# Kernel optimization log

Measured on AMD Instinct MI355X. Metric: run time of the kernel, lower is better.

## Reference

```python
import jax, jax.numpy as jnp
import numpy as np

GAMMA_MIN, GAMMA_MAX = 0.15, 1.0
ALPHA_CAP = 1.0
EPS_L2 = 1e-8
EPS_RMS = 1e-6


def _rmsnorm(x, w):
    return x * jax.lax.rsqrt(jnp.mean(x * x, axis=-1, keepdims=True) + EPS_RMS) * w


def _l2norm(x):
    n = jnp.linalg.norm(x, axis=-1, keepdims=True)
    return x / jnp.maximum(n, EPS_L2)


def _causal_conv(h, kernel):
    # depthwise-shared causal conv over time: out[b,t] = sum_j kernel[j] * h[b, t-j]
    K = kernel.shape[0]
    S = h.shape[1]
    hp = jnp.pad(h, ((0, 0), (K - 1, 0), (0, 0)))
    out = jnp.zeros_like(h)
    for j in range(K):  # K is a small fixed constant (4)
        out = out + kernel[j] * hp[:, K - 1 - j:K - 1 - j + S, :]
    return out


def setup_inputs() -> dict:
    B, S, D, R, K = 8, 1024, 1024, 16, 4
    key = jax.random.key(0)
    ks = jax.random.split(key, 8)
    return {
        'h': jax.random.normal(ks[0], (B, S, D), dtype=jnp.float32),
        'u': jax.random.normal(ks[1], (D, R), dtype=jnp.float32) * 0.05,
        'v': jax.random.normal(ks[2], (D, R), dtype=jnp.float32) * 0.05,
        'decay_logit': jnp.zeros((R,), jnp.float32),
        'alpha_logit': jnp.zeros((R,), jnp.float32),
        'k_base_gate_logit': jnp.float32(0.0),
        'k_base_kernel': jax.random.normal(ks[3], (K,), dtype=jnp.float32) * 0.05,
        'proj_w': jax.random.normal(ks[4], (D, D), dtype=jnp.float32) * 0.02,
        'proj_b': jnp.zeros((D,), jnp.float32),
        'norm1_w': jnp.ones((D,), jnp.float32),
        'norm2_w': jnp.ones((D,), jnp.float32),
        'mlp_w1': jax.random.normal(ks[5], (D, 4 * D), dtype=jnp.float32) * 0.02,
        'mlp_b1': jnp.zeros((4 * D,), jnp.float32),
        'mlp_w2': jax.random.normal(ks[6], (4 * D, D), dtype=jnp.float32) * 0.02,
        'mlp_b2': jnp.zeros((D,), jnp.float32),
    }


def reference(h, u, v, decay_logit, alpha_logit, k_base_gate_logit, k_base_kernel,
              proj_w, proj_b, norm1_w, norm2_w, mlp_w1, mlp_b1, mlp_w2, mlp_b2):
    B, S, D = h.shape
    R = u.shape[1]
    residual = h
    h_norm = _rmsnorm(h, norm1_w)

    # conv k_base term, gated
    gate = jax.nn.sigmoid(k_base_gate_logit)
    out = gate * _causal_conv(h_norm, k_base_kernel)

    # low-rank q/k projections
    alpha = ALPHA_CAP * jax.nn.sigmoid(alpha_logit)  # [R]
    qk = h_norm @ jnp.concatenate((u, v), axis=1)    # [B,S,2R]
    q_raw, k_raw = qk[..., :R], qk[..., R:]
    q = _l2norm(q_raw)
    k = _l2norm(k_raw)

    # per-rank causal decay matrix: w[r,i,j] = gamma[r]^(i-j) for i>=j else 0
    gamma = jnp.clip(jax.nn.sigmoid(decay_logit), GAMMA_MIN, GAMMA_MAX)  # [R]
    pos = jnp.arange(S, dtype=h.dtype)
    diff = jnp.maximum(pos[:, None] - pos[None, :], 0.0)   # [S,S]
    mask = jnp.tril(jnp.ones((S, S), dtype=h.dtype))
    w = (gamma[:, None, None] ** diff) * mask              # [R,S,S]

    q_alpha = q * alpha                                    # [B,S,R]
    A = jnp.einsum('bir,bjr,rij->bij', q_alpha, k, w)      # [B,S,S]
    decay_out = jnp.einsum('bij,bjd->bid', A, h_norm)      # [B,S,D]

    out = out + decay_out
    out = out @ proj_w.T + proj_b
    h2 = residual + out
    hn2 = _rmsnorm(h2, norm2_w)
    mlp_out = jax.nn.gelu(hn2 @ mlp_w1 + mlp_b1) @ mlp_w2 + mlp_b2
    return h2 + mlp_out
```

## Files before the change

kernel.cpp:

```cpp
#include <hip/hip_runtime.h>
#include <hip/hip_bf16.h>
#include <cstdint>
#include <cstddef>

typedef __bf16 bf16;
typedef __bf16 bf16x2 __attribute__((ext_vector_type(2)));
typedef __bf16 bf16x4 __attribute__((ext_vector_type(4)));
typedef __bf16 bf16x8 __attribute__((ext_vector_type(8)));
typedef float  floatx4 __attribute__((ext_vector_type(4)));

#define BB 8
#define SS 1024
#define DD 1024
#define RR 16
#define CHK 64
#define NCH 16

#define PP_ALPHA 0
#define PP_GAMMA 16
#define PP_GP    32
#define PP_KKER  (32 + 16*72)
#define PP_FLOATS 2048

__device__ __forceinline__ float sigmoidf_(float x) { return 1.0f / (1.0f + __expf(-x)); }

__device__ __forceinline__ float gelu_f(float x) {
    float u = 0.7978845608028654f * (x + 0.044715f * x * x * x);
    float t = 1.0f - 2.0f / (__expf(2.0f * u) + 1.0f);
    return 0.5f * x * (1.0f + t);
}

__device__ __forceinline__ void g2l16(const bf16* g, bf16* l) {
    __builtin_amdgcn_global_load_lds(
        (const __attribute__((address_space(1))) void*)g,
        (__attribute__((address_space(3))) void*)l, 16, 0, 0);
}

__global__ __launch_bounds__(256) void prep_kernel(
    const float* __restrict__ decay_logit, const float* __restrict__ alpha_logit,
    const float* __restrict__ gate_logit,  const float* __restrict__ kbase,
    const float* __restrict__ u, const float* __restrict__ v,
    const float* __restrict__ proj_w, const float* __restrict__ mlp_w1,
    const float* __restrict__ mlp_w2,
    float* __restrict__ pp, bf16* __restrict__ Ut, bf16* __restrict__ Wp,
    bf16* __restrict__ W1t, bf16* __restrict__ W2t) {
    __shared__ float tl[64][69];
    int t = threadIdx.x;
    int bid = blockIdx.x;
    if (bid == 0) {
        if (t < 16) {
            pp[PP_ALPHA + t] = sigmoidf_(alpha_logit[t]);
            float g = sigmoidf_(decay_logit[t]);
            g = fminf(fmaxf(g, 0.15f), 1.0f);
            pp[PP_GAMMA + t] = g;
            float acc = 1.0f;
            for (int p = 0; p < 72; ++p) { pp[PP_GP + t * 72 + p] = acc; acc *= g; }
        }
        if (t >= 16 && t < 20) {
            float gate = sigmoidf_(gate_logit[0]);
            pp[PP_KKER + (t - 16)] = gate * kbase[t - 16];
        }
        return;
    }
    if (bid < 33) {
        int c = bid - 1;
        const float* src = (c < 16) ? u : v;
        int cc = c & 15;
        for (int d = t; d < 1024; d += 256)
            Ut[c * 1024 + d] = (bf16)src[d * 16 + cc];
        return;
    }
    if (bid < 1057) {
        int i = (bid - 33) * 256 + t;
        float4 w = ((const float4*)proj_w)[i];
        bf16x4 o = { (bf16)w.x, (bf16)w.y, (bf16)w.z, (bf16)w.w };
        ((bf16x4*)Wp)[i] = o;
        return;
    }
    const float* in; bf16* outp; int K, N, tb;
    if (bid < 2081) { in = mlp_w1; outp = W1t; K = 1024; N = 4096; tb = bid - 1057; }
    else            { in = mlp_w2; outp = W2t; K = 4096; N = 1024; tb = bid - 2081; }
    int nx = N >> 6;
    int x0 = (tb % nx) * 64, y0 = (tb / nx) * 64;
    int tx = t & 15, ty = t >> 4;
    #pragma unroll
    for (int i = 0; i < 4; ++i) {
        float4 w = *(const float4*)(in + (size_t)(y0 + ty + i * 16) * N + x0 + tx * 4);
        tl[ty + i * 16][tx * 4 + 0] = w.x; tl[ty + i * 16][tx * 4 + 1] = w.y;
        tl[ty + i * 16][tx * 4 + 2] = w.z; tl[ty + i * 16][tx * 4 + 3] = w.w;
    }
    __syncthreads();
    #pragma unroll
    for (int i = 0; i < 4; ++i) {
        int nl = ty + i * 16;
        bf16x4 o = { (bf16)tl[tx * 4 + 0][nl], (bf16)tl[tx * 4 + 1][nl],
                     (bf16)tl[tx * 4 + 2][nl], (bf16)tl[tx * 4 + 3][nl] };
        *(bf16x4*)(outp + (size_t)(x0 + nl) * K + y0 + tx * 4) = o;
    }
}

__global__ __launch_bounds__(256) void rmsrow_kernel(
    const float* __restrict__ x, const float* __restrict__ nw, bf16* __restrict__ y) {
    __shared__ float red[4];
    int t = threadIdx.x;
    size_t row = blockIdx.x;
    float4 hv = ((const float4*)(x + row * DD))[t];
    float ss = hv.x*hv.x + hv.y*hv.y + hv.z*hv.z + hv.w*hv.w;
    for (int m = 32; m; m >>= 1) ss += __shfl_xor(ss, m);
    if ((t & 63) == 0) red[t >> 6] = ss;
    __syncthreads();
    float tot = red[0] + red[1] + red[2] + red[3];
    float rinv = rsqrtf(tot * (1.0f / 1024.0f) + 1e-6f);
    float4 wv = ((const float4*)nw)[t];
    bf16x4 o = { (bf16)(hv.x * rinv * wv.x), (bf16)(hv.y * rinv * wv.y),
                 (bf16)(hv.z * rinv * wv.z), (bf16)(hv.w * rinv * wv.w) };
    ((bf16x4*)(y + row * DD))[t] = o;
}

__global__ __launch_bounds__(256) void qk_kernel(
    const bf16* __restrict__ hn, const bf16* __restrict__ Ut,
    const float* __restrict__ pp, float* __restrict__ qa, float* __restrict__ kk) {
    __shared__ __attribute__((aligned(16))) bf16 As[32 * 64];
    __shared__ __attribute__((aligned(16))) bf16 Bs[32 * 64];
    int tid = threadIdx.x, lane = tid & 63, wid = tid >> 6;
    int quad = lane >> 4, l16 = lane & 15;
    int m0 = blockIdx.x * 32;
    int mt = wid >> 1, nt = wid & 1;
    int s_row = tid >> 3, s_cc = tid & 7;
    int s_gc = s_cc ^ (s_row & 7);
    const bf16* Ap = hn + (size_t)(m0 + s_row) * DD + s_gc * 8;
    const bf16* Bp = Ut + (size_t)s_row * DD + s_gc * 8;
    int slo = tid * 8;
    floatx4 acc = {};
    for (int kt = 0; kt < 1024; kt += 64) {
        g2l16(Ap + kt, As + slo);
        g2l16(Bp + kt, Bs + slo);
        __syncthreads();
        #pragma unroll
        for (int ks = 0; ks < 2; ++ks) {
            int arow = mt * 16 + l16;
            int acc_ = (ks * 4 + quad) ^ (arow & 7);
            bf16x8 af = *(const bf16x8*)(As + arow * 64 + acc_ * 8);
            int brow = nt * 16 + l16;
            int bcc = (ks * 4 + quad) ^ (brow & 7);
            bf16x8 bfr = *(const bf16x8*)(Bs + brow * 64 + bcc * 8);
            acc = __builtin_amdgcn_mfma_f32_16x16x32_bf16(af, bfr, acc, 0, 0, 0);
        }
        __syncthreads();
    }
    float alf = pp[PP_ALPHA + l16];
    float s2[4];
    #pragma unroll
    for (int r = 0; r < 4; ++r) s2[r] = acc[r] * acc[r];
    #pragma unroll
    for (int m = 1; m <= 8; m <<= 1)
        #pragma unroll
        for (int r = 0; r < 4; ++r) s2[r] += __shfl_xor(s2[r], m);
    #pragma unroll
    for (int r = 0; r < 4; ++r) {
        size_t row = m0 + mt * 16 + quad * 4 + r;
        float den = fmaxf(sqrtf(s2[r]), 1e-8f);
        float nvl = acc[r] / den;
        if (nt == 0) qa[row * RR + l16] = nvl * alf;
        else         kk[row * RR + l16] = nvl;
    }
}

__global__ __launch_bounds__(256) void incr_kernel(
    const bf16* __restrict__ hn, const float* __restrict__ kk,
    const float* __restrict__ pp, float* __restrict__ Inc) {
    __shared__ __attribute__((aligned(16))) float wjr[64][16];
    int t = threadIdx.x;
    int bc = blockIdx.x;
    int d0 = blockIdx.y * 512 + t * 2;
    size_t row0 = (size_t)bc * 64;
    for (int idx = t; idx < 1024; idx += 256) {
        int j = idx >> 4, r = idx & 15;
        wjr[j][r] = kk[(row0 + j) * RR + r] * pp[PP_GP + r * 72 + (63 - j)];
    }
    __syncthreads();
    float acc0[16] = {}, acc1[16] = {};
    for (int j = 0; j < 64; ++j) {
        bf16x2 hv = *(const bf16x2*)(hn + (row0 + j) * DD + d0);
        float x0 = (float)hv[0], x1 = (float)hv[1];
        const float4* w4 = (const float4*)wjr[j];
        #pragma unroll
        for (int g = 0; g < 4; ++g) {
            float4 w = w4[g];
            acc0[g*4+0] += w.x * x0; acc0[g*4+1] += w.y * x0;
            acc0[g*4+2] += w.z * x0; acc0[g*4+3] += w.w * x0;
            acc1[g*4+0] += w.x * x1; acc1[g*4+1] += w.y * x1;
            acc1[g*4+2] += w.z * x1; acc1[g*4+3] += w.w * x1;
        }
    }
    float* outp = Inc + (size_t)bc * 16 * 1024 + d0;
    #pragma unroll
    for (int r = 0; r < 16; ++r) {
        float2 o = { acc0[r], acc1[r] };
        *(float2*)&outp[r * 1024] = o;
    }
}

__global__ __launch_bounds__(256) void scan_kernel(
    const float* __restrict__ Inc, const float* __restrict__ pp,
    float* __restrict__ Sprev) {
    int gid = blockIdx.x * 256 + threadIdx.x;
    int b = gid >> 14, rd = gid & 16383;
    int r = rd >> 10;
    float gd = pp[PP_GP + r * 72 + 64];
    float s = 0.0f;
    for (int c = 0; c < 16; ++c) {
        size_t idx = ((size_t)(b * 16 + c) << 14) + rd;
        Sprev[idx] = s;
        s = s * gd + Inc[idx];
    }
}

#define XK 104
__global__ __launch_bounds__(256, 2) void phasec_kernel(
    const bf16* __restrict__ hn, const float* __restrict__ qa, const float* __restrict__ kk,
    const float* __restrict__ Sprev, const float* __restrict__ pp,
    bf16* __restrict__ outpre) {
    __shared__ __attribute__((aligned(16))) bf16 Xt[128][XK];
    __shared__ __attribute__((aligned(16))) bf16 Mb[64][XK];
    __shared__ __attribute__((aligned(16))) float qa_s[64][16];
    __shared__ __attribute__((aligned(16))) float kk_s[64][16];
    __shared__ __attribute__((aligned(16))) float gpt[65][16];
    __shared__ float kks[4];
    int t = threadIdx.x;
    int bc = blockIdx.x;
    int c = bc & 15;
    size_t row0 = (size_t)bc * 64;
    for (int idx = t; idx < 1024; idx += 256) {
        int j = idx >> 4, r = idx & 15;
        qa_s[j][r] = qa[(row0 + j) * RR + r];
        kk_s[j][r] = kk[(row0 + j) * RR + r];
    }
    for (int idx = t; idx < 16 * 65; idx += 256) {
        int p = idx >> 4, r = idx & 15;
        gpt[p][r] = pp[PP_GP + r * 72 + p];
    }
    if (t < 4) kks[t] = pp[PP_KKER + t];
    __syncthreads();
    for (int idx = t; idx < 64 * 96; idx += 256) {
        int ii = idx / 96, jj = idx - ii * 96;
        float val = 0.0f;
        if (jj < 64) {
            if (jj <= ii) {
                const float4* qa4 = (const float4*)qa_s[ii];
                const float4* kk4 = (const float4*)kk_s[jj];
                const float4* gp4 = (const float4*)gpt[ii - jj];
                float s = 0.0f;
                #pragma unroll
                for (int x = 0; x < 4; ++x) {
                    float4 qv = qa4[x], kv = kk4[x], gv = gp4[x];
                    s += qv.x*kv.x*gv.x + qv.y*kv.y*gv.y + qv.z*kv.z*gv.z + qv.w*kv.w*gv.w;
                }
                val = s;
                if (ii - jj <= 3) val += kks[ii - jj];
            }
        } else if (jj < 80) {
            int r = jj - 64;
            val = qa_s[ii][r] * gpt[ii + 1][r];
        } else if (jj < 83) {
            int p = jj - 80;
            if (ii <= p) val = kks[ii + 3 - p];
        }
        Mb[ii][jj] = (bf16)val;
    }
    int lane = t & 63, w = t >> 6, quad = lane >> 4, l16 = lane & 15;
    for (int it = 0; it < 2; ++it) {
        int dt = blockIdx.y * 256 + it * 128;
        __syncthreads();
        for (int idx = t; idx < 64 * 32; idx += 256) {
            int j = idx >> 5, ch = idx & 31;
            bf16x4 hv = *(const bf16x4*)(hn + (row0 + j) * DD + dt + ch * 4);
            #pragma unroll
            for (int ee = 0; ee < 4; ++ee) {
                int e = (ee + t) & 3;
                Xt[ch * 4 + e][j] = hv[e];
            }
        }
        for (int idx = t; idx < 16 * 128; idx += 256) {
            int r = idx >> 7, dd = idx & 127;
            Xt[dd][64 + r] = (bf16)Sprev[((size_t)bc << 14) + r * 1024 + dt + dd];
        }
        for (int idx = t; idx < 128 * 16; idx += 256) {
            int dd = idx >> 4, p = idx & 15;
            bf16 val = (bf16)0.0f;
            if (p < 3 && c > 0) val = hn[(row0 - 3 + p) * DD + dt + dd];
            Xt[dd][80 + p] = val;
        }
        __syncthreads();
        floatx4 acc[8] = {};
        #pragma unroll
        for (int ks = 0; ks < 3; ++ks) {
            bf16x8 af = *(const bf16x8*)(&Mb[w * 16 + l16][ks * 32 + quad * 8]);
            #pragma unroll
            for (int tn = 0; tn < 8; ++tn) {
                bf16x8 bfr = *(const bf16x8*)(&Xt[tn * 16 + l16][ks * 32 + quad * 8]);
                acc[tn] = __builtin_amdgcn_mfma_f32_16x16x32_bf16(af, bfr, acc[tn], 0, 0, 0);
            }
        }
        #pragma unroll
        for (int tn = 0; tn < 8; ++tn) {
            #pragma unroll
            for (int r = 0; r < 4; ++r) {
                size_t ii = w * 16 + quad * 4 + r;
                outpre[(row0 + ii) * DD + dt + tn * 16 + l16] = (bf16)acc[tn][r];
            }
        }
    }
}

template <int EPI, int BK>
__global__ __launch_bounds__(256, 2) void gemm_bt_kernel(
    const bf16* __restrict__ A, const bf16* __restrict__ Bt,
    const float* __restrict__ bias, const float* __restrict__ resid,
    float* __restrict__ outf, bf16* __restrict__ outb, int K, int N) {
    constexpr int CH = BK / 8;
    constexpr int PT = 128 * CH / 256;
    __shared__ __attribute__((aligned(16))) bf16 As[128 * BK];
    __shared__ __attribute__((aligned(16))) bf16 Bs[128 * BK];
    int tid = threadIdx.x, lane = tid & 63, wid = tid >> 6;
    int quad = lane >> 4, l16 = lane & 15;
    int lb = blockIdx.y * gridDim.x + blockIdx.x;
    int xcd = lb & 7, q = lb >> 3;
    int m0 = (xcd * 8 + (q & 7)) * 128;
    int n0 = (q >> 3) * 128;
    int wm = (wid >> 1) * 64, wn = (wid & 1) * 64;
    const bf16* Ap[PT]; const bf16* Bp[PT]; int lo[PT];
    #pragma unroll
    for (int j = 0; j < PT; ++j) {
        int s = j * 256 + tid;
        int row = s / CH, cc = s % CH;
        int gc = cc ^ (row & (CH - 1));
        Ap[j] = A  + (size_t)(m0 + row) * K + gc * 8;
        Bp[j] = Bt + (size_t)(n0 + row) * K + gc * 8;
        lo[j] = s * 8;
    }
    floatx4 acc[4][4] = {};
    for (int kt = 0; kt < K; kt += BK) {
        #pragma unroll
        for (int j = 0; j < PT; ++j) {
            g2l16(Ap[j] + kt, As + lo[j]);
            g2l16(Bp[j] + kt, Bs + lo[j]);
        }
        __syncthreads();
        #pragma unroll
        for (int ks = 0; ks < BK / 32; ++ks) {
            bf16x8 af[4], bfr[4];
            #pragma unroll
            for (int tm = 0; tm < 4; ++tm) {
                int row = wm + tm * 16 + l16;
                int cc = (ks * 4 + quad) ^ (row & (CH - 1));
                af[tm] = *(const bf16x8*)(As + row * BK + cc * 8);
            }
            #pragma unroll
            for (int tn = 0; tn < 4; ++tn) {
                int row = wn + tn * 16 + l16;
                int cc = (ks * 4 + quad) ^ (row & (CH - 1));
                bfr[tn] = *(const bf16x8*)(Bs + row * BK + cc * 8);
            }
            #pragma unroll
            for (int tm = 0; tm < 4; ++tm)
                #pragma unroll
                for (int tn = 0; tn < 4; ++tn)
                    acc[tm][tn] = __builtin_amdgcn_mfma_f32_16x16x32_bf16(
                        af[tm], bfr[tn], acc[tm][tn], 0, 0, 0);
        }
        __syncthreads();
    }
    #pragma unroll
    for (int tn = 0; tn < 4; ++tn) {
        int gn = n0 + wn + tn * 16 + l16;
        float bs = bias[gn];
        #pragma unroll
        for (int tm = 0; tm < 4; ++tm) {
            #pragma unroll
            for (int r = 0; r < 4; ++r) {
                size_t gm = (size_t)m0 + wm + tm * 16 + quad * 4 + r;
                float v = acc[tm][tn][r] + bs;
                if (EPI == 1) {
                    outb[gm * N + gn] = (bf16)gelu_f(v);
                } else {
                    v += resid[gm * N + gn];
                    outf[gm * N + gn] = v;
                }
            }
        }
    }
}

extern "C" void kernel_launch(void* const* d_in, const int* in_sizes, int n_in,
                              void* d_out, int out_size, void* d_ws, size_t ws_size,
                              hipStream_t stream) {
    const float* h           = (const float*)d_in[0];
    const float* u           = (const float*)d_in[1];
    const float* v           = (const float*)d_in[2];
    const float* decay_logit = (const float*)d_in[3];
    const float* alpha_logit = (const float*)d_in[4];
    const float* gate_logit  = (const float*)d_in[5];
    const float* kbase       = (const float*)d_in[6];
    const float* proj_w      = (const float*)d_in[7];
    const float* proj_b      = (const float*)d_in[8];
    const float* norm1_w     = (const float*)d_in[9];
    const float* norm2_w     = (const float*)d_in[10];
    const float* mlp_w1      = (const float*)d_in[11];
    const float* mlp_b1      = (const float*)d_in[12];
    const float* mlp_w2      = (const float*)d_in[13];
    const float* mlp_b2      = (const float*)d_in[14];
    float* out = (float*)d_out;

    char* wsb = (char*)d_ws;
    size_t off = 0;
    auto alloc = [&](size_t bytes) -> void* {
        void* p = wsb + off;
        off += (bytes + 255) & ~(size_t)255;
        return p;
    };
    float* pp     = (float*)alloc(PP_FLOATS * 4);
    bf16*  Ut     = (bf16*) alloc((size_t)32 * 1024 * 2);
    bf16*  hn     = (bf16*) alloc((size_t)8192 * 1024 * 2);
    float* qa     = (float*)alloc((size_t)8192 * 16 * 4);
    float* kk     = (float*)alloc((size_t)8192 * 16 * 4);
    float* Inc    = (float*)alloc((size_t)128 * 16 * 1024 * 4);
    float* Sprev  = (float*)alloc((size_t)128 * 16 * 1024 * 4);
    bf16*  outpre = (bf16*) alloc((size_t)8192 * 1024 * 2);
    float* h2     = (float*)alloc((size_t)8192 * 1024 * 4);
    bf16*  hidden = (bf16*) alloc((size_t)8192 * 4096 * 2);
    bf16*  Wp     = (bf16*) alloc((size_t)1024 * 1024 * 2);
    bf16*  W1t    = (bf16*) alloc((size_t)4096 * 1024 * 2);
    bf16*  W2t    = (bf16*) alloc((size_t)1024 * 4096 * 2);
    bf16*  hn2 = hn;

    prep_kernel<<<3105, 256, 0, stream>>>(decay_logit, alpha_logit, gate_logit, kbase,
                                          u, v, proj_w, mlp_w1, mlp_w2,
                                          pp, Ut, Wp, W1t, W2t);
    rmsrow_kernel<<<8192, 256, 0, stream>>>(h, norm1_w, hn);
    qk_kernel<<<256, 256, 0, stream>>>(hn, Ut, pp, qa, kk);
    incr_kernel<<<dim3(128, 2), 256, 0, stream>>>(hn, kk, pp, Inc);
    scan_kernel<<<512, 256, 0, stream>>>(Inc, pp, Sprev);
    phasec_kernel<<<dim3(128, 4), 256, 0, stream>>>(hn, qa, kk, Sprev, pp, outpre);
    gemm_bt_kernel<0, 128><<<dim3(8, 64), 256, 0, stream>>>(outpre, Wp, proj_b, h, h2, nullptr, 1024, 1024);
    rmsrow_kernel<<<8192, 256, 0, stream>>>(h2, norm2_w, hn2);
    gemm_bt_kernel<1, 64><<<dim3(32, 64), 256, 0, stream>>>(hn2, W1t, mlp_b1, nullptr, nullptr, hidden, 1024, 4096);
    gemm_bt_kernel<2, 128><<<dim3(8, 64), 256, 0, stream>>>(hidden, W2t, mlp_b2, h2, out, nullptr, 4096, 1024);
}
```

Before: 374.8 us.

## Fuse first RMSNorm into prep, store h2 and Sprev as bf16, stage GELU epilogue

```diff
diff --git a/kernel.cpp b/kernel.cpp
--- a/kernel.cpp
+++ b/kernel.cpp
@@ -37,17 +37,35 @@
 }
 
 __global__ __launch_bounds__(256) void prep_kernel(
+    const float* __restrict__ h, const float* __restrict__ norm1_w,
     const float* __restrict__ decay_logit, const float* __restrict__ alpha_logit,
     const float* __restrict__ gate_logit,  const float* __restrict__ kbase,
     const float* __restrict__ u, const float* __restrict__ v,
     const float* __restrict__ proj_w, const float* __restrict__ mlp_w1,
     const float* __restrict__ mlp_w2,
-    float* __restrict__ pp, bf16* __restrict__ Ut, bf16* __restrict__ Wp,
-    bf16* __restrict__ W1t, bf16* __restrict__ W2t) {
+    float* __restrict__ pp, bf16* __restrict__ hn, bf16* __restrict__ Ut,
+    bf16* __restrict__ Wp, bf16* __restrict__ W1t, bf16* __restrict__ W2t) {
     __shared__ float tl[64][69];
+    __shared__ float red[4];
     int t = threadIdx.x;
     int bid = blockIdx.x;
-    if (bid == 0) {
+    if (bid < 8192) {
+        size_t row = bid;
+        float4 hv = ((const float4*)(h + row * DD))[t];
+        float ss = hv.x*hv.x + hv.y*hv.y + hv.z*hv.z + hv.w*hv.w;
+        for (int m = 32; m; m >>= 1) ss += __shfl_xor(ss, m);
+        if ((t & 63) == 0) red[t >> 6] = ss;
+        __syncthreads();
+        float tot = red[0] + red[1] + red[2] + red[3];
+        float rinv = rsqrtf(tot * (1.0f / 1024.0f) + 1e-6f);
+        float4 wv = ((const float4*)norm1_w)[t];
+        bf16x4 o = { (bf16)(hv.x * rinv * wv.x), (bf16)(hv.y * rinv * wv.y),
+                     (bf16)(hv.z * rinv * wv.z), (bf16)(hv.w * rinv * wv.w) };
+        ((bf16x4*)(hn + row * DD))[t] = o;
+        return;
+    }
+    int b2 = bid - 8192;
+    if (b2 == 0) {
         if (t < 16) {
             pp[PP_ALPHA + t] = sigmoidf_(alpha_logit[t]);
             float g = sigmoidf_(decay_logit[t]);
@@ -62,24 +80,24 @@
         }
         return;
     }
-    if (bid < 33) {
-        int c = bid - 1;
+    if (b2 < 33) {
+        int c = b2 - 1;
         const float* src = (c < 16) ? u : v;
         int cc = c & 15;
         for (int d = t; d < 1024; d += 256)
             Ut[c * 1024 + d] = (bf16)src[d * 16 + cc];
         return;
     }
-    if (bid < 1057) {
-        int i = (bid - 33) * 256 + t;
+    if (b2 < 1057) {
+        int i = (b2 - 33) * 256 + t;
         float4 w = ((const float4*)proj_w)[i];
         bf16x4 o = { (bf16)w.x, (bf16)w.y, (bf16)w.z, (bf16)w.w };
         ((bf16x4*)Wp)[i] = o;
         return;
     }
     const float* in; bf16* outp; int K, N, tb;
-    if (bid < 2081) { in = mlp_w1; outp = W1t; K = 1024; N = 4096; tb = bid - 1057; }
-    else            { in = mlp_w2; outp = W2t; K = 4096; N = 1024; tb = bid - 2081; }
+    if (b2 < 2081) { in = mlp_w1; outp = W1t; K = 1024; N = 4096; tb = b2 - 1057; }
+    else           { in = mlp_w2; outp = W2t; K = 4096; N = 1024; tb = b2 - 2081; }
     int nx = N >> 6;
     int x0 = (tb % nx) * 64, y0 = (tb / nx) * 64;
     int tx = t & 15, ty = t >> 4;
@@ -99,51 +117,60 @@
     }
 }
 
-__global__ __launch_bounds__(256) void rmsrow_kernel(
-    const float* __restrict__ x, const float* __restrict__ nw, bf16* __restrict__ y) {
+__global__ __launch_bounds__(256) void rms2b_kernel(
+    const bf16* __restrict__ x, const float* __restrict__ nw, bf16* __restrict__ y) {
     __shared__ float red[4];
     int t = threadIdx.x;
     size_t row = blockIdx.x;
-    float4 hv = ((const float4*)(x + row * DD))[t];
-    float ss = hv.x*hv.x + hv.y*hv.y + hv.z*hv.z + hv.w*hv.w;
+    bf16x4 hv = ((const bf16x4*)(x + row * DD))[t];
+    float x0 = (float)hv[0], x1 = (float)hv[1], x2 = (float)hv[2], x3 = (float)hv[3];
+    float ss = x0*x0 + x1*x1 + x2*x2 + x3*x3;
     for (int m = 32; m; m >>= 1) ss += __shfl_xor(ss, m);
     if ((t & 63) == 0) red[t >> 6] = ss;
     __syncthreads();
     float tot = red[0] + red[1] + red[2] + red[3];
     float rinv = rsqrtf(tot * (1.0f / 1024.0f) + 1e-6f);
     float4 wv = ((const float4*)nw)[t];
-    bf16x4 o = { (bf16)(hv.x * rinv * wv.x), (bf16)(hv.y * rinv * wv.y),
-                 (bf16)(hv.z * rinv * wv.z), (bf16)(hv.w * rinv * wv.w) };
+    bf16x4 o = { (bf16)(x0 * rinv * wv.x), (bf16)(x1 * rinv * wv.y),
+                 (bf16)(x2 * rinv * wv.z), (bf16)(x3 * rinv * wv.w) };
     ((bf16x4*)(y + row * DD))[t] = o;
 }
 
 __global__ __launch_bounds__(256) void qk_kernel(
     const bf16* __restrict__ hn, const bf16* __restrict__ Ut,
     const float* __restrict__ pp, float* __restrict__ qa, float* __restrict__ kk) {
-    __shared__ __attribute__((aligned(16))) bf16 As[32 * 64];
-    __shared__ __attribute__((aligned(16))) bf16 Bs[32 * 64];
+    __shared__ __attribute__((aligned(16))) bf16 As[32 * 128];
+    __shared__ __attribute__((aligned(16))) bf16 Bs[32 * 128];
     int tid = threadIdx.x, lane = tid & 63, wid = tid >> 6;
     int quad = lane >> 4, l16 = lane & 15;
     int m0 = blockIdx.x * 32;
     int mt = wid >> 1, nt = wid & 1;
-    int s_row = tid >> 3, s_cc = tid & 7;
-    int s_gc = s_cc ^ (s_row & 7);
-    const bf16* Ap = hn + (size_t)(m0 + s_row) * DD + s_gc * 8;
-    const bf16* Bp = Ut + (size_t)s_row * DD + s_gc * 8;
-    int slo = tid * 8;
+    const bf16* Ap[2]; const bf16* Bp[2]; int lo[2];
+    #pragma unroll
+    for (int j = 0; j < 2; ++j) {
+        int s = j * 256 + tid;
+        int row = s >> 4, cc = s & 15;
+        int gc = cc ^ (row & 15);
+        Ap[j] = hn + (size_t)(m0 + row) * DD + gc * 8;
+        Bp[j] = Ut + (size_t)row * DD + gc * 8;
+        lo[j] = s * 8;
+    }
     floatx4 acc = {};
-    for (int kt = 0; kt < 1024; kt += 64) {
-        g2l16(Ap + kt, As + slo);
-        g2l16(Bp + kt, Bs + slo);
-        __syncthreads();
-        #pragma unroll
-        for (int ks = 0; ks < 2; ++ks) {
+    for (int kt = 0; kt < 1024; kt += 128) {
+        #pragma unroll
+        for (int j = 0; j < 2; ++j) {
+            g2l16(Ap[j] + kt, As + lo[j]);
+            g2l16(Bp[j] + kt, Bs + lo[j]);
+        }
+        __syncthreads();
+        #pragma unroll
+        for (int ks = 0; ks < 4; ++ks) {
             int arow = mt * 16 + l16;
-            int acc_ = (ks * 4 + quad) ^ (arow & 7);
-            bf16x8 af = *(const bf16x8*)(As + arow * 64 + acc_ * 8);
+            int acc_ = (ks * 4 + quad) ^ (arow & 15);
+            bf16x8 af = *(const bf16x8*)(As + arow * 128 + acc_ * 8);
             int brow = nt * 16 + l16;
-            int bcc = (ks * 4 + quad) ^ (brow & 7);
-            bf16x8 bfr = *(const bf16x8*)(Bs + brow * 64 + bcc * 8);
+            int bcc = (ks * 4 + quad) ^ (brow & 15);
+            bf16x8 bfr = *(const bf16x8*)(Bs + brow * 128 + bcc * 8);
             acc = __builtin_amdgcn_mfma_f32_16x16x32_bf16(af, bfr, acc, 0, 0, 0);
         }
         __syncthreads();
@@ -203,7 +230,7 @@
 
 __global__ __launch_bounds__(256) void scan_kernel(
     const float* __restrict__ Inc, const float* __restrict__ pp,
-    float* __restrict__ Sprev) {
+    bf16* __restrict__ Sprevb) {
     int gid = blockIdx.x * 256 + threadIdx.x;
     int b = gid >> 14, rd = gid & 16383;
     int r = rd >> 10;
@@ -211,7 +238,7 @@
     float s = 0.0f;
     for (int c = 0; c < 16; ++c) {
         size_t idx = ((size_t)(b * 16 + c) << 14) + rd;
-        Sprev[idx] = s;
+        Sprevb[idx] = (bf16)s;
         s = s * gd + Inc[idx];
     }
 }
@@ -219,7 +246,7 @@
 #define XK 104
 __global__ __launch_bounds__(256, 2) void phasec_kernel(
     const bf16* __restrict__ hn, const float* __restrict__ qa, const float* __restrict__ kk,
-    const float* __restrict__ Sprev, const float* __restrict__ pp,
+    const bf16* __restrict__ Sprevb, const float* __restrict__ pp,
     bf16* __restrict__ outpre) {
     __shared__ __attribute__((aligned(16))) bf16 Xt[128][XK];
     __shared__ __attribute__((aligned(16))) bf16 Mb[64][XK];
@@ -283,7 +310,7 @@
         }
         for (int idx = t; idx < 16 * 128; idx += 256) {
             int r = idx >> 7, dd = idx & 127;
-            Xt[dd][64 + r] = (bf16)Sprev[((size_t)bc << 14) + r * 1024 + dt + dd];
+            Xt[dd][64 + r] = Sprevb[((size_t)bc << 14) + r * 1024 + dt + dd];
         }
         for (int idx = t; idx < 128 * 16; idx += 256) {
             int dd = idx >> 4, p = idx & 15;
@@ -316,12 +343,14 @@
 template <int EPI, int BK>
 __global__ __launch_bounds__(256, 2) void gemm_bt_kernel(
     const bf16* __restrict__ A, const bf16* __restrict__ Bt,
-    const float* __restrict__ bias, const float* __restrict__ resid,
-    float* __restrict__ outf, bf16* __restrict__ outb, int K, int N) {
+    const float* __restrict__ bias, const float* __restrict__ residf,
+    const bf16* __restrict__ residb, float* __restrict__ outf,
+    bf16* __restrict__ outb, int K, int N) {
     constexpr int CH = BK / 8;
     constexpr int PT = 128 * CH / 256;
-    __shared__ __attribute__((aligned(16))) bf16 As[128 * BK];
-    __shared__ __attribute__((aligned(16))) bf16 Bs[128 * BK];
+    __shared__ __attribute__((aligned(16))) bf16 smem[128 * BK * 2];
+    bf16* As = smem;
+    bf16* Bs = smem + 128 * BK;
     int tid = threadIdx.x, lane = tid & 63, wid = tid >> 6;
     int quad = lane >> 4, l16 = lane & 15;
     int lb = blockIdx.y * gridDim.x + blockIdx.x;
@@ -371,21 +400,50 @@
         }
         __syncthreads();
     }
-    #pragma unroll
-    for (int tn = 0; tn < 4; ++tn) {
-        int gn = n0 + wn + tn * 16 + l16;
-        float bs = bias[gn];
-        #pragma unroll
-        for (int tm = 0; tm < 4; ++tm) {
-            #pragma unroll
-            for (int r = 0; r < 4; ++r) {
-                size_t gm = (size_t)m0 + wm + tm * 16 + quad * 4 + r;
-                float v = acc[tm][tn][r] + bs;
-                if (EPI == 1) {
-                    outb[gm * N + gn] = (bf16)gelu_f(v);
-                } else {
-                    v += resid[gm * N + gn];
-                    outf[gm * N + gn] = v;
+    if (EPI == 1) {
+        bf16 (*Cs)[136] = (bf16 (*)[136])smem;
+        #pragma unroll
+        for (int p = 0; p < 2; ++p) {
+            if ((wid >> 1) == p) {
+                #pragma unroll
+                for (int tn = 0; tn < 4; ++tn) {
+                    int cl = wn + tn * 16 + l16;
+                    float bs = bias[n0 + cl];
+                    #pragma unroll
+                    for (int tm = 0; tm < 4; ++tm)
+                        #pragma unroll
+                        for (int r = 0; r < 4; ++r)
+                            Cs[tm * 16 + quad * 4 + r][cl] =
+                                (bf16)gelu_f(acc[tm][tn][r] + bs);
+                }
+            }
+            __syncthreads();
+            int row = tid >> 2, cg = (tid & 3) * 32;
+            const bf16* src = &Cs[row][cg];
+            bf16* dst = outb + (size_t)(m0 + p * 64 + row) * N + n0 + cg;
+            #pragma unroll
+            for (int x = 0; x < 4; ++x)
+                *(bf16x8*)(dst + x * 8) = *(const bf16x8*)(src + x * 8);
+            __syncthreads();
+        }
+    } else {
+        #pragma unroll
+        for (int tn = 0; tn < 4; ++tn) {
+            int gn = n0 + wn + tn * 16 + l16;
+            float bs = bias[gn];
+            #pragma unroll
+            for (int tm = 0; tm < 4; ++tm) {
+                #pragma unroll
+                for (int r = 0; r < 4; ++r) {
+                    size_t gm = (size_t)m0 + wm + tm * 16 + quad * 4 + r;
+                    float v = acc[tm][tn][r] + bs;
+                    if (EPI == 0) {
+                        v += residf[gm * N + gn];
+                        outb[gm * N + gn] = (bf16)v;
+                    } else {
+                        v += (float)residb[gm * N + gn];
+                        outf[gm * N + gn] = v;
+                    }
                 }
             }
         }
@@ -425,25 +483,27 @@
     float* qa     = (float*)alloc((size_t)8192 * 16 * 4);
     float* kk     = (float*)alloc((size_t)8192 * 16 * 4);
     float* Inc    = (float*)alloc((size_t)128 * 16 * 1024 * 4);
-    float* Sprev  = (float*)alloc((size_t)128 * 16 * 1024 * 4);
+    bf16*  Sprevb = (bf16*) alloc((size_t)128 * 16 * 1024 * 2);
     bf16*  outpre = (bf16*) alloc((size_t)8192 * 1024 * 2);
-    float* h2     = (float*)alloc((size_t)8192 * 1024 * 4);
+    bf16*  h2b    = (bf16*) alloc((size_t)8192 * 1024 * 2);
     bf16*  hidden = (bf16*) alloc((size_t)8192 * 4096 * 2);
     bf16*  Wp     = (bf16*) alloc((size_t)1024 * 1024 * 2);
     bf16*  W1t    = (bf16*) alloc((size_t)4096 * 1024 * 2);
     bf16*  W2t    = (bf16*) alloc((size_t)1024 * 4096 * 2);
     bf16*  hn2 = hn;
 
-    prep_kernel<<<3105, 256, 0, stream>>>(decay_logit, alpha_logit, gate_logit, kbase,
-                                          u, v, proj_w, mlp_w1, mlp_w2,
-                                          pp, Ut, Wp, W1t, W2t);
-    rmsrow_kernel<<<8192, 256, 0, stream>>>(h, norm1_w, hn);
+    prep_kernel<<<8192 + 3105, 256, 0, stream>>>(
+        h, norm1_w, decay_logit, alpha_logit, gate_logit, kbase,
+        u, v, proj_w, mlp_w1, mlp_w2, pp, hn, Ut, Wp, W1t, W2t);
     qk_kernel<<<256, 256, 0, stream>>>(hn, Ut, pp, qa, kk);
     incr_kernel<<<dim3(128, 2), 256, 0, stream>>>(hn, kk, pp, Inc);
-    scan_kernel<<<512, 256, 0, stream>>>(Inc, pp, Sprev);
-    phasec_kernel<<<dim3(128, 4), 256, 0, stream>>>(hn, qa, kk, Sprev, pp, outpre);
-    gemm_bt_kernel<0, 128><<<dim3(8, 64), 256, 0, stream>>>(outpre, Wp, proj_b, h, h2, nullptr, 1024, 1024);
-    rmsrow_kernel<<<8192, 256, 0, stream>>>(h2, norm2_w, hn2);
-    gemm_bt_kernel<1, 64><<<dim3(32, 64), 256, 0, stream>>>(hn2, W1t, mlp_b1, nullptr, nullptr, hidden, 1024, 4096);
-    gemm_bt_kernel<2, 128><<<dim3(8, 64), 256, 0, stream>>>(hidden, W2t, mlp_b2, h2, out, nullptr, 4096, 1024);
-}
+    scan_kernel<<<512, 256, 0, stream>>>(Inc, pp, Sprevb);
+    phasec_kernel<<<dim3(128, 4), 256, 0, stream>>>(hn, qa, kk, Sprevb, pp, outpre);
+    gemm_bt_kernel<0, 128><<<dim3(8, 64), 256, 0, stream>>>(
+        outpre, Wp, proj_b, h, nullptr, nullptr, h2b, 1024, 1024);
+    rms2b_kernel<<<8192, 256, 0, stream>>>(h2b, norm2_w, hn2);
+    gemm_bt_kernel<1, 64><<<dim3(32, 64), 256, 0, stream>>>(
+        hn2, W1t, mlp_b1, nullptr, nullptr, nullptr, hidden, 1024, 4096);
+    gemm_bt_kernel<2, 128><<<dim3(8, 64), 256, 0, stream>>>(
+        hidden, W2t, mlp_b2, nullptr, h2b, out, nullptr, 4096, 1024);
+}
```

Measured after the change: 387.9 us. +3.5%, slower.
